# Optimization experiments

Hardware: AMD Instinct MI355X
Metric: run time of the kernel (lower is better)

The kernel has to match this reference:

```python
import jax, jax.numpy as jnp
import numpy as np

B, C, H, W = 8, 256, 128, 128
KC, VC, HEADS = 256, 256, 8


def setup_inputs() -> dict:
    key = jax.random.key(0)
    ks = jax.random.split(key, 10)
    s = 0.05
    return {
        "x": jax.random.normal(ks[0], (B, C, H, W), jnp.float32),
        "Wk": jax.random.normal(ks[1], (KC, C), jnp.float32) * s,
        "bk": jax.random.normal(ks[2], (KC,), jnp.float32) * s,
        "Wq": jax.random.normal(ks[3], (KC, C), jnp.float32) * s,
        "bq": jax.random.normal(ks[4], (KC,), jnp.float32) * s,
        "Wv": jax.random.normal(ks[5], (VC, C), jnp.float32) * s,
        "bv": jax.random.normal(ks[6], (VC,), jnp.float32) * s,
        "Wr": jax.random.normal(ks[7], (C, VC), jnp.float32) * s,
        "br": jax.random.normal(ks[8], (C,), jnp.float32) * s,
        "head_count": HEADS,
    }


def reference(x, Wk, bk, Wq, bq, Wv, bv, Wr, br, head_count):
    n, c, h, w = x.shape
    hw = h * w
    xf = x.reshape(n, c, hw)  # [n, C, S]
    # 1x1 convs == per-pixel linear projections
    keys = jnp.einsum('kc,ncs->nks', Wk, xf) + bk[None, :, None]
    queries = jnp.einsum('kc,ncs->nks', Wq, xf) + bq[None, :, None]
    values = jnp.einsum('vc,ncs->nvs', Wv, xf) + bv[None, :, None]

    dk = Wk.shape[0] // head_count
    dv = Wv.shape[0] // head_count
    # split heads along channel dim (matches torch channel slicing)
    K = jax.nn.softmax(keys.reshape(n, head_count, dk, hw), axis=-1)   # softmax over spatial
    Q = jax.nn.softmax(queries.reshape(n, head_count, dk, hw), axis=2) # softmax over key dim
    V = values.reshape(n, head_count, dv, hw)

    # context = K @ V^T : [n, h, dk, dv]
    ctx = jnp.einsum('nhks,nhvs->nhkv', K, V)
    # attended = ctx^T @ Q : [n, h, dv, S]
    att = jnp.einsum('nhkv,nhks->nhvs', ctx, Q).reshape(n, head_count * dv, h, w)

    attention = jnp.einsum('ov,nvhw->nohw', Wr, att) + br[None, :, None, None]
    # attention map: per-head mean over key dim, then mean over heads
    attention_map = K.mean(axis=2).mean(axis=1).reshape(n, h, w)
    # torch returns the LAST head's context (loop variable after the loop)
    context_last = ctx[:, -1]
    return attention, context_last, attention_map
```

## Files before the change

### kernel.cpp

```cpp
#include <hip/hip_runtime.h>
#include <hip/hip_bf16.h>

typedef float f32x4 __attribute__((ext_vector_type(4)));
typedef short s16x8 __attribute__((ext_vector_type(8)));
typedef __bf16 bf16x8 __attribute__((ext_vector_type(8)));
typedef unsigned short u16;

#define DEVI __device__ __forceinline__

static constexpr int    HW      = 16384;
static constexpr size_t BSTRIDE = (size_t)256 * HW;

static constexpr size_t oXBT   = 0;
static constexpr size_t oEK    = oXBT  + (size_t)8 * HW * 256 * 2;
static constexpr size_t oQT    = oEK   + (size_t)8 * 256 * HW * 2;
static constexpr size_t oVB    = oQT   + (size_t)8 * HW * 256 * 2;
static constexpr size_t oWK    = oVB   + (size_t)8 * 256 * HW * 2;
static constexpr size_t oBIAS  = oWK   + (size_t)768 * 256 * 2;
static constexpr size_t oISE   = oBIAS + 4096;
static constexpr size_t oPS    = oISE  + 8192;
static constexpr size_t oCTX   = oPS   + (size_t)256 * 2048 * 4;
static constexpr size_t oMB    = oCTX  + (size_t)64 * 1024 * 4;
static constexpr size_t oCPART = oMB   + (size_t)8 * 256 * 256 * 2;
static constexpr size_t oMPART = oCPART + (size_t)4096 * 1024 * 4;

DEVI float bf2f(short x) {
  unsigned u = ((unsigned)(unsigned short)x) << 16;
  return __builtin_bit_cast(float, u);
}
DEVI u16 f2bf(float x) { return __builtin_bit_cast(u16, (__bf16)x); }

DEVI void gld16(const void* g, void* l) {
  __builtin_amdgcn_global_load_lds(
      (__attribute__((address_space(1))) void*)(g),
      (__attribute__((address_space(3))) void*)(l), 16, 0, 0);
}

__global__ __launch_bounds__(256) void k_prep(
    const float* __restrict__ Wk, const float* __restrict__ Wq, const float* __restrict__ Wv,
    const float* __restrict__ bk, const float* __restrict__ bq, const float* __restrict__ bv,
    u16* __restrict__ Wkqv, float* __restrict__ bias)
{
  int i = blockIdx.x * 256 + threadIdx.x;
  for (int p = i; p < 768 * 256; p += 64 * 256) {
    float v = (p < 65536) ? Wk[p] : (p < 131072 ? Wq[p - 65536] : Wv[p - 131072]);
    Wkqv[p] = f2bf(v);
  }
  if (i < 768) bias[i] = (i < 256) ? bk[i] : (i < 512 ? bq[i - 256] : bv[i - 512]);
}

__global__ __launch_bounds__(256) void k_transpose(const float* __restrict__ in_, u16* __restrict__ out)
{
  __shared__ u16 lds[64 * 256];
  const int t = threadIdx.x;
  const int n = blockIdx.y;
  const int s0 = blockIdx.x * 64;
  const float* src = in_ + ((size_t)n * 256 + t) * HW + s0;
  #pragma unroll
  for (int i = 0; i < 16; ++i) {
    f32x4 v = *(const f32x4*)(src + i * 4);
    #pragma unroll
    for (int j = 0; j < 4; ++j) lds[(i * 4 + j) * 256 + t] = f2bf(v[j]);
  }
  __syncthreads();
  s16x8* gp = (s16x8*)(out + (size_t)n * BSTRIDE + (size_t)s0 * 256);
  const s16x8* lp = (const s16x8*)lds;
  #pragma unroll
  for (int i = 0; i < 8; ++i) gp[t + i * 256] = lp[t + i * 256];
}

__global__ __launch_bounds__(256) void k_proj(
    const u16* __restrict__ W, const u16* __restrict__ xbT, const float* __restrict__ bias,
    u16* __restrict__ ek, u16* __restrict__ qT, u16* __restrict__ vb, float* __restrict__ ps)
{
  __shared__ u16 smem[17408];
  u16* Al = smem;
  u16* Bl = smem + 8192;
  const int t = threadIdx.x;
  const int L = blockIdx.x;
  const int n  = L & 7;
  const int idx = L >> 3;
  const int mb = idx % 6;
  const int sb = idx / 6;
  const int m0 = mb * 128, s0 = sb * 128;
  const int lane = t & 63;
  const int l15 = lane & 15, l4 = lane >> 4;
  const int wv = t >> 6;
  const int wm = (wv & 1) * 64, wn = (wv >> 1) * 64;
  const u16* Ab = W + (size_t)m0 * 256;
  const u16* Bb = xbT + (size_t)n * BSTRIDE + (size_t)s0 * 256;
  const int ar = t >> 2, ac = (t & 3) * 8;

  f32x4 acc[4][4] = {};

  auto stage = [&](int buf, int k0) {
    gld16(Ab + (size_t)ar * 256 + k0 + ac,        Al + buf * 4096 + t * 8);
    gld16(Ab + (size_t)(ar + 64) * 256 + k0 + ac, Al + buf * 4096 + 2048 + t * 8);
    gld16(Bb + (size_t)ar * 256 + k0 + ac,        Bl + buf * 4096 + t * 8);
    gld16(Bb + (size_t)(ar + 64) * 256 + k0 + ac, Bl + buf * 4096 + 2048 + t * 8);
  };

  stage(0, 0);
  __syncthreads();
  #pragma unroll
  for (int kt = 0; kt < 8; ++kt) {
    const int buf = kt & 1;
    if (kt < 7) stage(buf ^ 1, (kt + 1) * 32);
    bf16x8 af[4], bff[4];
    #pragma unroll
    for (int g = 0; g < 4; ++g) {
      af[g]  = *(const bf16x8*)&Al[buf * 4096 + (wm + g * 16 + l15) * 32 + l4 * 8];
      bff[g] = *(const bf16x8*)&Bl[buf * 4096 + (wn + g * 16 + l15) * 32 + l4 * 8];
    }
    #pragma unroll
    for (int mg = 0; mg < 4; ++mg)
      #pragma unroll
      for (int ng = 0; ng < 4; ++ng)
        acc[mg][ng] = __builtin_amdgcn_mfma_f32_16x16x32_bf16(af[mg], bff[ng], acc[mg][ng], 0, 0, 0);
    __syncthreads();
  }

  #pragma unroll
  for (int mg = 0; mg < 4; ++mg)
    #pragma unroll
    for (int r = 0; r < 4; ++r) {
      const float bb = bias[m0 + wm + mg * 16 + l4 * 4 + r];
      #pragma unroll
      for (int ng = 0; ng < 4; ++ng) acc[mg][ng][r] += bb;
    }

  const int rowBase = (mb & 1) * 128;

  if (mb < 2) {
    #pragma unroll
    for (int mg = 0; mg < 4; ++mg)
      #pragma unroll
      for (int r = 0; r < 4; ++r) {
        float s_ = 0.f;
        #pragma unroll
        for (int ng = 0; ng < 4; ++ng) {
          const float e = __expf(acc[mg][ng][r]);
          acc[mg][ng][r] = e; s_ += e;
        }
        s_ += __shfl_xor(s_, 1); s_ += __shfl_xor(s_, 2);
        s_ += __shfl_xor(s_, 4); s_ += __shfl_xor(s_, 8);
        if (l15 == 0) {
          const int row = rowBase + wm + mg * 16 + l4 * 4 + r;
          ps[((size_t)(sb * 2 + (wn >> 6))) * 2048 + n * 256 + row] = s_;
        }
      }
    u16* O = ek + (size_t)n * BSTRIDE;
    #pragma unroll
    for (int mg = 0; mg < 4; ++mg)
      #pragma unroll
      for (int r = 0; r < 4; ++r) {
        const size_t row = rowBase + wm + mg * 16 + l4 * 4 + r;
        u16* op = O + row * HW + s0 + wn + l15;
        #pragma unroll
        for (int ng = 0; ng < 4; ++ng) op[ng * 16] = f2bf(acc[mg][ng][r]);
      }
  } else if (mb < 4) {
    #pragma unroll
    for (int hh = 0; hh < 2; ++hh)
      #pragma unroll
      for (int ng = 0; ng < 4; ++ng) {
        float s = 0.f;
        #pragma unroll
        for (int mg = hh * 2; mg < hh * 2 + 2; ++mg)
          #pragma unroll
          for (int r = 0; r < 4; ++r) { const float e = __expf(acc[mg][ng][r]); acc[mg][ng][r] = e; s += e; }
        s += __shfl_xor(s, 16);
        s += __shfl_xor(s, 32);
        const float inv = 1.f / s;
        #pragma unroll
        for (int mg = hh * 2; mg < hh * 2 + 2; ++mg)
          #pragma unroll
          for (int r = 0; r < 4; ++r) acc[mg][ng][r] *= inv;
      }
    #pragma unroll
    for (int mg = 0; mg < 4; ++mg)
      #pragma unroll
      for (int ng = 0; ng < 4; ++ng)
        #pragma unroll
        for (int r = 0; r < 4; ++r) {
          const int srow = wn + ng * 16 + l15;
          const int mcol = wm + mg * 16 + l4 * 4 + r;
          smem[srow * 136 + mcol] = f2bf(acc[mg][ng][r]);
        }
    __syncthreads();
    u16* O = qT + (size_t)n * BSTRIDE + (size_t)s0 * 256 + rowBase;
    #pragma unroll
    for (int it = 0; it < 8; ++it) {
      const int row = it * 16 + (t >> 4);
      *(s16x8*)(O + (size_t)row * 256 + (t & 15) * 8) = *(const s16x8*)&smem[row * 136 + (t & 15) * 8];
    }
  } else {
    u16* O = vb + (size_t)n * BSTRIDE;
    #pragma unroll
    for (int mg = 0; mg < 4; ++mg)
      #pragma unroll
      for (int r = 0; r < 4; ++r) {
        const size_t row = rowBase + wm + mg * 16 + l4 * 4 + r;
        u16* op = O + row * HW + s0 + wn + l15;
        #pragma unroll
        for (int ng = 0; ng < 4; ++ng) op[ng * 16] = f2bf(acc[mg][ng][r]);
      }
  }
}

__global__ __launch_bounds__(256) void k_inv(const float* __restrict__ ps, float* __restrict__ ise)
{
  const int i = blockIdx.x * 256 + threadIdx.x;
  float s = 0.f;
  for (int b = 0; b < 256; ++b) s += ps[(size_t)b * 2048 + i];
  ise[i] = 1.f / s;
}

__global__ __launch_bounds__(64) void k_ctx_part(
    const u16* __restrict__ ek, const u16* __restrict__ vb, const float* __restrict__ ise,
    float* __restrict__ cpart, float* __restrict__ mpart)
{
  const int blk = blockIdx.x;
  const int chunk = blk & 63, nh = blk >> 6;
  const int h = nh & 7, n = nh >> 3;
  const int lane = threadIdx.x;
  const int l15 = lane & 15, l4 = lane >> 4;
  const u16* kb = ek + ((size_t)n * 256 + h * 32) * HW;
  const u16* vv = vb + ((size_t)n * 256 + h * 32) * HW;
  const float iv0 = ise[n * 256 + h * 32 + l15];
  const float iv1 = ise[n * 256 + h * 32 + 16 + l15];
  f32x4 acc[2][2] = {};
  float macc[8][8] = {};
  const int sbase = chunk * 256 + l4 * 8;
  #pragma unroll
  for (int ks = 0; ks < 8; ++ks) {
    const int sb = sbase + ks * 32;
    bf16x8 ef[2], vf[2];
    #pragma unroll
    for (int g = 0; g < 2; ++g) {
      ef[g] = *(const bf16x8*)(kb + (size_t)(g * 16 + l15) * HW + sb);
// ... 50 lines not shown
  if (h == 7) *(f32x4*)(dctx + (size_t)n * 1024 + t * 4) = a;
}

__global__ __launch_bounds__(256) void k_mmat(
    const float* __restrict__ ctx, const float* __restrict__ Wr, u16* __restrict__ Mb)
{
  const int nh = blockIdx.x, n = nh >> 3, h = nh & 7, o = threadIdx.x;
  __shared__ float cl[1024];
  #pragma unroll
  for (int i = 0; i < 4; ++i) cl[o + i * 256] = ctx[(size_t)nh * 1024 + o + i * 256];
  __syncthreads();
  float wr[32];
  const float* wp = Wr + (size_t)o * 256 + h * 32;
  #pragma unroll
  for (int v = 0; v < 32; ++v) wr[v] = wp[v];
  u16* mp = Mb + ((size_t)n * 256 + o) * 256 + h * 32;
  #pragma unroll 4
  for (int k = 0; k < 32; ++k) {
    float s = 0.f;
    #pragma unroll
    for (int v = 0; v < 32; ++v) s += wr[v] * cl[k * 32 + v];
    mp[k] = f2bf(s);
  }
}

__global__ __launch_bounds__(256) void k_map_reduce(const float* __restrict__ mpart, float* __restrict__ dmap)
{
  const int i = blockIdx.x * 256 + threadIdx.x;
  f32x4 a = {};
  #pragma unroll
  for (int h = 0; h < 8; ++h) a += *(const f32x4*)(mpart + (size_t)h * 131072 + (size_t)i * 4);
  a *= (1.0f / 256.0f);
  *(f32x4*)(dmap + (size_t)i * 4) = a;
}

__global__ __launch_bounds__(256) void k_attn(
    const u16* __restrict__ Mb, const u16* __restrict__ qT, const float* __restrict__ br,
    float* __restrict__ Out)
{
  __shared__ u16 Al[2][4096];
  __shared__ u16 Bl[2][4096];
  const int t = threadIdx.x;
  const int L = blockIdx.x;
  const int n = L & 7;
  const int idx = L >> 3;
  const int m0 = (idx & 1) * 128;
  const int s0 = (idx >> 1) * 128;
  const int lane = t & 63;
  const int l15 = lane & 15, l4 = lane >> 4;
  const int wv = t >> 6;
  const int wm = (wv & 1) * 64, wn = (wv >> 1) * 64;
  const u16* Ab = Mb + (size_t)n * 65536 + (size_t)m0 * 256;
  const u16* Bb = qT + (size_t)n * BSTRIDE + (size_t)s0 * 256;
  const int ar = t >> 2, ac = (t & 3) * 8;

  f32x4 acc[4][4] = {};

  auto stage = [&](int buf, int k0) {
    gld16(Ab + (size_t)ar * 256 + k0 + ac,        &Al[buf][t * 8]);
    gld16(Ab + (size_t)(ar + 64) * 256 + k0 + ac, &Al[buf][2048 + t * 8]);
    gld16(Bb + (size_t)ar * 256 + k0 + ac,        &Bl[buf][t * 8]);
    gld16(Bb + (size_t)(ar + 64) * 256 + k0 + ac, &Bl[buf][2048 + t * 8]);
  };

  stage(0, 0);
  __syncthreads();
  #pragma unroll
  for (int kt = 0; kt < 8; ++kt) {
    const int buf = kt & 1;
    if (kt < 7) stage(buf ^ 1, (kt + 1) * 32);
    bf16x8 af[4], bff[4];
    #pragma unroll
    for (int g = 0; g < 4; ++g) {
      af[g]  = *(const bf16x8*)&Al[buf][(wm + g * 16 + l15) * 32 + l4 * 8];
      bff[g] = *(const bf16x8*)&Bl[buf][(wn + g * 16 + l15) * 32 + l4 * 8];
    }
    #pragma unroll
    for (int mg = 0; mg < 4; ++mg)
      #pragma unroll
      for (int ng = 0; ng < 4; ++ng)
        acc[mg][ng] = __builtin_amdgcn_mfma_f32_16x16x32_bf16(af[mg], bff[ng], acc[mg][ng], 0, 0, 0);
    __syncthreads();
  }

  float* O = Out + (size_t)n * BSTRIDE;
  #pragma unroll
  for (int mg = 0; mg < 4; ++mg)
    #pragma unroll
    for (int r = 0; r < 4; ++r) {
      const size_t row = m0 + wm + mg * 16 + l4 * 4 + r;
      const float bb = br[row];
      float* op = O + row * HW + s0 + wn + l15;
      #pragma unroll
      for (int ng = 0; ng < 4; ++ng) op[ng * 16] = acc[mg][ng][r] + bb;
    }
}

extern "C" void kernel_launch(void* const* d_in, const int* in_sizes, int n_in,
                              void* d_out, int out_size, void* d_ws, size_t ws_size,
                              hipStream_t stream)
{
  (void)in_sizes; (void)n_in; (void)out_size; (void)ws_size;
  const float* x  = (const float*)d_in[0];
  const float* Wk = (const float*)d_in[1];
  const float* bk = (const float*)d_in[2];
  const float* Wq = (const float*)d_in[3];
  const float* bq = (const float*)d_in[4];
  const float* Wv = (const float*)d_in[5];
  const float* bv = (const float*)d_in[6];
  const float* Wr = (const float*)d_in[7];
  const float* br = (const float*)d_in[8];

  char* ws = (char*)d_ws;
  u16*   xbT  = (u16*)(ws + oXBT);
  u16*   ek   = (u16*)(ws + oEK);
  u16*   qT   = (u16*)(ws + oQT);
  u16*   vb   = (u16*)(ws + oVB);
  u16*   Wkqv = (u16*)(ws + oWK);
  float* bias = (float*)(ws + oBIAS);
  float* ise  = (float*)(ws + oISE);
  float* ps   = (float*)(ws + oPS);
  float* ctx  = (float*)(ws + oCTX);
  u16*   Mb   = (u16*)(ws + oMB);
  float* cpart= (float*)(ws + oCPART);
  float* mpart= (float*)(ws + oMPART);

  float* attn = (float*)d_out;
  float* dctx = (float*)d_out + 33554432;
  float* dmap = (float*)d_out + 33562624;

  k_prep<<<64, 256, 0, stream>>>(Wk, Wq, Wv, bk, bq, bv, Wkqv, bias);
  k_transpose<<<dim3(256, 8), 256, 0, stream>>>(x, xbT);
  k_proj<<<6144, 256, 0, stream>>>(Wkqv, xbT, bias, ek, qT, vb, ps);
  k_inv<<<8, 256, 0, stream>>>(ps, ise);
  k_ctx_part<<<4096, 64, 0, stream>>>(ek, vb, ise, cpart, mpart);
  k_ctx_reduce<<<64, 256, 0, stream>>>(cpart, ise, ctx, dctx);
  k_mmat<<<64, 256, 0, stream>>>(ctx, Wr, Mb);
  k_map_reduce<<<128, 256, 0, stream>>>(mpart, dmap);
  k_attn<<<2048, 256, 0, stream>>>(Mb, qT, br, attn);
}
```

Measured before the change: 289.7 us.

## Replace projection and output GEMMs with 256x256-tile templated kernel with swizzled LDS

```diff
diff --git a/kernel.cpp b/kernel.cpp
--- a/kernel.cpp
+++ b/kernel.cpp
@@ -3,6 +3,7 @@
 
 typedef float f32x4 __attribute__((ext_vector_type(4)));
 typedef short s16x8 __attribute__((ext_vector_type(8)));
+typedef short s16x4 __attribute__((ext_vector_type(4)));
 typedef __bf16 bf16x8 __attribute__((ext_vector_type(8)));
 typedef unsigned short u16;
 
@@ -36,6 +37,8 @@
       (__attribute__((address_space(3))) void*)(l), 16, 0, 0);
 }
 
+DEVI void cfence() { asm volatile("" ::: "memory"); }
+
 __global__ __launch_bounds__(256) void k_prep(
     const float* __restrict__ Wk, const float* __restrict__ Wq, const float* __restrict__ Wv,
     const float* __restrict__ bk, const float* __restrict__ bq, const float* __restrict__ bv,
@@ -69,142 +72,186 @@
   for (int i = 0; i < 8; ++i) gp[t + i * 256] = lp[t + i * 256];
 }
 
-__global__ __launch_bounds__(256) void k_proj(
-    const u16* __restrict__ W, const u16* __restrict__ xbT, const float* __restrict__ bias,
-    u16* __restrict__ ek, u16* __restrict__ qT, u16* __restrict__ vb, float* __restrict__ ps)
-{
-  __shared__ u16 smem[17408];
-  u16* Al = smem;
-  u16* Bl = smem + 8192;
+template<int MODE>
+__global__ __launch_bounds__(512, 2) void k_gemm256(
+    const u16* __restrict__ A, const u16* __restrict__ B, const float* __restrict__ bias,
+    u16* __restrict__ o_ek, u16* __restrict__ o_qT, u16* __restrict__ o_vb,
+    float* __restrict__ o_ps, float* __restrict__ o_f32)
+{
+  __shared__ u16 smem[65536];
   const int t = threadIdx.x;
   const int L = blockIdx.x;
-  const int n  = L & 7;
+  const int n = L & 7;
   const int idx = L >> 3;
-  const int mb = idx % 6;
-  const int sb = idx / 6;
-  const int m0 = mb * 128, s0 = sb * 128;
+  int mb, sb;
+  if constexpr (MODE == 0) { mb = idx % 3; sb = idx / 3; }
+  else                     { mb = 0;       sb = idx; }
+  const int s0 = sb * 256;
   const int lane = t & 63;
   const int l15 = lane & 15, l4 = lane >> 4;
-  const int wv = t >> 6;
-  const int wm = (wv & 1) * 64, wn = (wv >> 1) * 64;
-  const u16* Ab = W + (size_t)m0 * 256;
-  const u16* Bb = xbT + (size_t)n * BSTRIDE + (size_t)s0 * 256;
-  const int ar = t >> 2, ac = (t & 3) * 8;
-
-  f32x4 acc[4][4] = {};
-
-  auto stage = [&](int buf, int k0) {
-    gld16(Ab + (size_t)ar * 256 + k0 + ac,        Al + buf * 4096 + t * 8);
-    gld16(Ab + (size_t)(ar + 64) * 256 + k0 + ac, Al + buf * 4096 + 2048 + t * 8);
-    gld16(Bb + (size_t)ar * 256 + k0 + ac,        Bl + buf * 4096 + t * 8);
-    gld16(Bb + (size_t)(ar + 64) * 256 + k0 + ac, Bl + buf * 4096 + 2048 + t * 8);
+  const int w = t >> 6;
+  const int wr = w & 1, wc = w >> 1;
+  const int tr = t >> 3;
+  const int csw = (t & 7) ^ (tr & 7);
+
+  const u16* Ag = A + (MODE == 0 ? (size_t)mb * 65536 : (size_t)n * 65536);
+  const u16* Bg = B + (size_t)n * BSTRIDE + (size_t)s0 * 256;
+
+  auto STAGE = [&](int buf, int kt) {
+    const int k0 = kt * 64 + csw * 8;
+    #pragma unroll
+    for (int i = 0; i < 4; ++i) {
+      const size_t r = (size_t)(i * 64 + tr);
+      gld16(Ag + r * 256 + k0, smem + buf * 16384 + (i * 512 + t) * 8);
+      gld16(Bg + r * 256 + k0, smem + 32768 + buf * 16384 + (i * 512 + t) * 8);
+    }
   };
 
-  stage(0, 0);
+  f32x4 acc[8][4] = {};
+
+  auto COMPUTE = [&](int buf) {
+    const u16* Al = smem + buf * 16384;
+    const u16* Bl = smem + 32768 + buf * 16384;
+    bf16x8 bf[4][2];
+    #pragma unroll
+    for (int b = 0; b < 4; ++b) {
+      const int s = wc * 64 + b * 16 + l15;
+      #pragma unroll
+      for (int ks = 0; ks < 2; ++ks)
+        bf[b][ks] = *(const bf16x8*)&Bl[s * 64 + ((ks * 4 + l4) ^ (s & 7)) * 8];
+    }
+    #pragma unroll
+    for (int p = 0; p < 4; ++p) {
+      bf16x8 af[2][2];
+      #pragma unroll
+      for (int a2 = 0; a2 < 2; ++a2) {
+        const int m = wr * 128 + (p * 2 + a2) * 16 + l15;
+        #pragma unroll
+        for (int ks = 0; ks < 2; ++ks)
+          af[a2][ks] = *(const bf16x8*)&Al[m * 64 + ((ks * 4 + l4) ^ (m & 7)) * 8];
+      }
+      __builtin_amdgcn_s_setprio(1);
+      #pragma unroll
+      for (int a2 = 0; a2 < 2; ++a2)
+        #pragma unroll
+        for (int b = 0; b < 4; ++b)
+          #pragma unroll
+          for (int ks = 0; ks < 2; ++ks)
+            acc[p * 2 + a2][b] = __builtin_amdgcn_mfma_f32_16x16x32_bf16(
+                af[a2][ks], bf[b][ks], acc[p * 2 + a2][b], 0, 0, 0);
+      __builtin_amdgcn_s_setprio(0);
+    }
+  };
+
+  STAGE(0, 0); STAGE(1, 1);
+  #pragma unroll
+  for (int kt = 0; kt < 4; ++kt) {
+    if (kt < 3) asm volatile("s_waitcnt vmcnt(8)" ::: "memory");
+    else        asm volatile("s_waitcnt vmcnt(0)" ::: "memory");
+    cfence(); __builtin_amdgcn_s_barrier(); cfence();
+    COMPUTE(kt & 1);
+    asm volatile("s_waitcnt lgkmcnt(0)" ::: "memory");
+    cfence(); __builtin_amdgcn_s_barrier(); cfence();
+    if (kt < 2) STAGE(kt & 1, kt + 2);
+  }
   __syncthreads();
-  #pragma unroll
-  for (int kt = 0; kt < 8; ++kt) {
-    const int buf = kt & 1;
-    if (kt < 7) stage(buf ^ 1, (kt + 1) * 32);
-    bf16x8 af[4], bff[4];
-    #pragma unroll
-    for (int g = 0; g < 4; ++g) {
-      af[g]  = *(const bf16x8*)&Al[buf * 4096 + (wm + g * 16 + l15) * 32 + l4 * 8];
-      bff[g] = *(const bf16x8*)&Bl[buf * 4096 + (wn + g * 16 + l15) * 32 + l4 * 8];
-    }
-    #pragma unroll
-    for (int mg = 0; mg < 4; ++mg)
-      #pragma unroll
-      for (int ng = 0; ng < 4; ++ng)
-        acc[mg][ng] = __builtin_amdgcn_mfma_f32_16x16x32_bf16(af[mg], bff[ng], acc[mg][ng], 0, 0, 0);
-    __syncthreads();
-  }
-
-  #pragma unroll
-  for (int mg = 0; mg < 4; ++mg)
-    #pragma unroll
-    for (int r = 0; r < 4; ++r) {
-      const float bb = bias[m0 + wm + mg * 16 + l4 * 4 + r];
-      #pragma unroll
-      for (int ng = 0; ng < 4; ++ng) acc[mg][ng][r] += bb;
-    }
-
-  const int rowBase = (mb & 1) * 128;
-
-  if (mb < 2) {
-    #pragma unroll
-    for (int mg = 0; mg < 4; ++mg)
+
+  if constexpr (MODE == 1) {
+    float* O = o_f32 + (size_t)n * BSTRIDE;
+    #pragma unroll
+    for (int am = 0; am < 8; ++am)
       #pragma unroll
       for (int r = 0; r < 4; ++r) {
-        float s_ = 0.f;
-        #pragma unroll
-        for (int ng = 0; ng < 4; ++ng) {
-          const float e = __expf(acc[mg][ng][r]);
-          acc[mg][ng][r] = e; s_ += e;
-        }
+        const int m = wr * 128 + am * 16 + l4 * 4 + r;
+        const float bb = bias[m];
+        float* op = O + (size_t)m * HW + s0 + wc * 64 + l15;
+        #pragma unroll
+        for (int b = 0; b < 4; ++b) op[b * 16] = acc[am][b][r] + bb;
+      }
+    return;
+  } else {
+  if (mb == 0) {
+    float* psrow = o_ps + ((size_t)(sb * 4 + wc) * 8 + n) * 256;
+    u16* O = o_ek + (size_t)n * BSTRIDE;
+    #pragma unroll
+    for (int am = 0; am < 8; ++am)
+      #pragma unroll
+      for (int r = 0; r < 4; ++r) {
+        const int m = wr * 128 + am * 16 + l4 * 4 + r;
+        const float bb = bias[m];
+        const float e0 = __expf(acc[am][0][r] + bb), e1 = __expf(acc[am][1][r] + bb);
+        const float e2 = __expf(acc[am][2][r] + bb), e3 = __expf(acc[am][3][r] + bb);
+        float s_ = e0 + e1 + e2 + e3;
         s_ += __shfl_xor(s_, 1); s_ += __shfl_xor(s_, 2);
         s_ += __shfl_xor(s_, 4); s_ += __shfl_xor(s_, 8);
-        if (l15 == 0) {
-          const int row = rowBase + wm + mg * 16 + l4 * 4 + r;
-          ps[((size_t)(sb * 2 + (wn >> 6))) * 2048 + n * 256 + row] = s_;
-        }
-      }
-    u16* O = ek + (size_t)n * BSTRIDE;
-    #pragma unroll
-    for (int mg = 0; mg < 4; ++mg)
+        if (l15 == 0) psrow[m] = s_;
+        u16* op = O + (size_t)m * HW + s0 + wc * 64 + l15;
+        op[0] = f2bf(e0); op[16] = f2bf(e1); op[32] = f2bf(e2); op[48] = f2bf(e3);
+      }
+  } else if (mb == 1) {
+    #pragma unroll
+    for (int am = 0; am < 8; ++am)
       #pragma unroll
       for (int r = 0; r < 4; ++r) {
-        const size_t row = rowBase + wm + mg * 16 + l4 * 4 + r;
-        u16* op = O + row * HW + s0 + wn + l15;
-        #pragma unroll
-        for (int ng = 0; ng < 4; ++ng) op[ng * 16] = f2bf(acc[mg][ng][r]);
-      }
-  } else if (mb < 4) {
-    #pragma unroll
-    for (int hh = 0; hh < 2; ++hh)
-      #pragma unroll
-      for (int ng = 0; ng < 4; ++ng) {
+        const float bb = bias[256 + wr * 128 + am * 16 + l4 * 4 + r];
+        #pragma unroll
+        for (int b = 0; b < 4; ++b) acc[am][b][r] += bb;
+      }
+    #pragma unroll
+    for (int hh = 0; hh < 4; ++hh)
+      #pragma unroll
+      for (int b = 0; b < 4; ++b) {
         float s = 0.f;
         #pragma unroll
-        for (int mg = hh * 2; mg < hh * 2 + 2; ++mg)
+        for (int a2 = 0; a2 < 2; ++a2)
           #pragma unroll
-          for (int r = 0; r < 4; ++r) { const float e = __expf(acc[mg][ng][r]); acc[mg][ng][r] = e; s += e; }
-        s += __shfl_xor(s, 16);
-        s += __shfl_xor(s, 32);
+          for (int r = 0; r < 4; ++r) {
+            const float e = __expf(acc[hh * 2 + a2][b][r]);
+            acc[hh * 2 + a2][b][r] = e; s += e;
+          }
+        s += __shfl_xor(s, 16); s += __shfl_xor(s, 32);
         const float inv = 1.f / s;
         #pragma unroll
-        for (int mg = hh * 2; mg < hh * 2 + 2; ++mg)
+        for (int a2 = 0; a2 < 2; ++a2)
           #pragma unroll
-          for (int r = 0; r < 4; ++r) acc[mg][ng][r] *= inv;
-      }
-    #pragma unroll
-    for (int mg = 0; mg < 4; ++mg)
-      #pragma unroll
-      for (int ng = 0; ng < 4; ++ng)
-        #pragma unroll
-        for (int r = 0; r < 4; ++r) {
-          const int srow = wn + ng * 16 + l15;
-          const int mcol = wm + mg * 16 + l4 * 4 + r;
-          smem[srow * 136 + mcol] = f2bf(acc[mg][ng][r]);
-        }
-    __syncthreads();
-    u16* O = qT + (size_t)n * BSTRIDE + (size_t)s0 * 256 + rowBase;
-    #pragma unroll
-    for (int it = 0; it < 8; ++it) {
-      const int row = it * 16 + (t >> 4);
-      *(s16x8*)(O + (size_t)row * 256 + (t & 15) * 8) = *(const s16x8*)&smem[row * 136 + (t & 15) * 8];
+          for (int r = 0; r < 4; ++r) acc[hh * 2 + a2][b][r] *= inv;
+      }
+    #pragma unroll
+    for (int H = 0; H < 2; ++H) {
+      if ((wc >> 1) == H) {
+        #pragma unroll
+        for (int am = 0; am < 8; ++am)
+          #pragma unroll
+          for (int b = 0; b < 4; ++b) {
+            const int srow = wc * 64 + b * 16 + l15 - H * 128;
+            s16x4 pk;
+            #pragma unroll
+            for (int r = 0; r < 4; ++r) pk[r] = (short)f2bf(acc[am][b][r]);
+            *(s16x4*)&smem[srow * 264 + wr * 128 + am * 16 + l4 * 4] = pk;
+          }
+      }
+      __syncthreads();
+      const int row = t >> 2;
+      const int cq = (t & 3) * 64;
+      u16* dst = o_qT + (size_t)n * BSTRIDE + (size_t)(s0 + H * 128 + row) * 256 + cq;
+      const u16* srcl = smem + row * 264 + cq;
+      #pragma unroll
+      for (int i = 0; i < 8; ++i) *(s16x8*)(dst + i * 8) = *(const s16x8*)(srcl + i * 8);
+      __syncthreads();
     }
   } else {
-    u16* O = vb + (size_t)n * BSTRIDE;
-    #pragma unroll
-    for (int mg = 0; mg < 4; ++mg)
+    u16* O = o_vb + (size_t)n * BSTRIDE;
+    #pragma unroll
+    for (int am = 0; am < 8; ++am)
       #pragma unroll
       for (int r = 0; r < 4; ++r) {
-        const size_t row = rowBase + wm + mg * 16 + l4 * 4 + r;
-        u16* op = O + row * HW + s0 + wn + l15;
-        #pragma unroll
-        for (int ng = 0; ng < 4; ++ng) op[ng * 16] = f2bf(acc[mg][ng][r]);
-      }
+        const int m = wr * 128 + am * 16 + l4 * 4 + r;
+        const float bb = bias[512 + m];
+        u16* op = O + (size_t)m * HW + s0 + wc * 64 + l15;
+        #pragma unroll
+        for (int b = 0; b < 4; ++b) op[b * 16] = f2bf(acc[am][b][r] + bb);
+      }
+  }
   }
 }
 
@@ -322,68 +369,6 @@
   for (int h = 0; h < 8; ++h) a += *(const f32x4*)(mpart + (size_t)h * 131072 + (size_t)i * 4);
   a *= (1.0f / 256.0f);
   *(f32x4*)(dmap + (size_t)i * 4) = a;
-}
-
-__global__ __launch_bounds__(256) void k_attn(
-    const u16* __restrict__ Mb, const u16* __restrict__ qT, const float* __restrict__ br,
-    float* __restrict__ Out)
-{
-  __shared__ u16 Al[2][4096];
-  __shared__ u16 Bl[2][4096];
-  const int t = threadIdx.x;
-  const int L = blockIdx.x;
-  const int n = L & 7;
-  const int idx = L >> 3;
-  const int m0 = (idx & 1) * 128;
-  const int s0 = (idx >> 1) * 128;
-  const int lane = t & 63;
-  const int l15 = lane & 15, l4 = lane >> 4;
-  const int wv = t >> 6;
-  const int wm = (wv & 1) * 64, wn = (wv >> 1) * 64;
-  const u16* Ab = Mb + (size_t)n * 65536 + (size_t)m0 * 256;
-  const u16* Bb = qT + (size_t)n * BSTRIDE + (size_t)s0 * 256;
-  const int ar = t >> 2, ac = (t & 3) * 8;
-
-  f32x4 acc[4][4] = {};
-
-  auto stage = [&](int buf, int k0) {
-    gld16(Ab + (size_t)ar * 256 + k0 + ac,        &Al[buf][t * 8]);
-    gld16(Ab + (size_t)(ar + 64) * 256 + k0 + ac, &Al[buf][2048 + t * 8]);
-    gld16(Bb + (size_t)ar * 256 + k0 + ac,        &Bl[buf][t * 8]);
-    gld16(Bb + (size_t)(ar + 64) * 256 + k0 + ac, &Bl[buf][2048 + t * 8]);
-  };
-
-  stage(0, 0);
-  __syncthreads();
-  #pragma unroll
-  for (int kt = 0; kt < 8; ++kt) {
-    const int buf = kt & 1;
-    if (kt < 7) stage(buf ^ 1, (kt + 1) * 32);
-    bf16x8 af[4], bff[4];
-    #pragma unroll
-    for (int g = 0; g < 4; ++g) {
-      af[g]  = *(const bf16x8*)&Al[buf][(wm + g * 16 + l15) * 32 + l4 * 8];
-      bff[g] = *(const bf16x8*)&Bl[buf][(wn + g * 16 + l15) * 32 + l4 * 8];
-    }
-    #pragma unroll
-    for (int mg = 0; mg < 4; ++mg)
-      #pragma unroll
-      for (int ng = 0; ng < 4; ++ng)
-        acc[mg][ng] = __builtin_amdgcn_mfma_f32_16x16x32_bf16(af[mg], bff[ng], acc[mg][ng], 0, 0, 0);
-    __syncthreads();
-  }
-
-  float* O = Out + (size_t)n * BSTRIDE;
-  #pragma unroll
-  for (int mg = 0; mg < 4; ++mg)
-    #pragma unroll
-    for (int r = 0; r < 4; ++r) {
-      const size_t row = m0 + wm + mg * 16 + l4 * 4 + r;
-      const float bb = br[row];
-      float* op = O + row * HW + s0 + wn + l15;
-      #pragma unroll
-      for (int ng = 0; ng < 4; ++ng) op[ng * 16] = acc[mg][ng][r] + bb;
-    }
 }
 
 extern "C" void kernel_launch(void* const* d_in, const int* in_sizes, int n_in,
@@ -421,11 +406,11 @@
 
   k_prep<<<64, 256, 0, stream>>>(Wk, Wq, Wv, bk, bq, bv, Wkqv, bias);
   k_transpose<<<dim3(256, 8), 256, 0, stream>>>(x, xbT);
-  k_proj<<<6144, 256, 0, stream>>>(Wkqv, xbT, bias, ek, qT, vb, ps);
+  k_gemm256<0><<<1536, 512, 0, stream>>>(Wkqv, xbT, bias, ek, qT, vb, ps, nullptr);
   k_inv<<<8, 256, 0, stream>>>(ps, ise);
   k_ctx_part<<<4096, 64, 0, stream>>>(ek, vb, ise, cpart, mpart);
   k_ctx_reduce<<<64, 256, 0, stream>>>(cpart, ise, ctx, dctx);
   k_mmat<<<64, 256, 0, stream>>>(ctx, Wr, Mb);
   k_map_reduce<<<128, 256, 0, stream>>>(mpart, dmap);
-  k_attn<<<2048, 256, 0, stream>>>(Mb, qT, br, attn);
-}
+  k_gemm256<1><<<512, 512, 0, stream>>>(Mb, qT, br, nullptr, nullptr, nullptr, nullptr, attn);
+}
```

Measured after the change: 316.6 us. 1.09x slower.

## Unify projection and output GEMMs into persistent multi-tile kernel with swizzled LDS

Applied to the files above, without the earlier changes.

```diff
diff --git a/kernel.cpp b/kernel.cpp
--- a/kernel.cpp
+++ b/kernel.cpp
@@ -3,6 +3,7 @@
 
 typedef float f32x4 __attribute__((ext_vector_type(4)));
 typedef short s16x8 __attribute__((ext_vector_type(8)));
+typedef short s16x4 __attribute__((ext_vector_type(4)));
 typedef __bf16 bf16x8 __attribute__((ext_vector_type(8)));
 typedef unsigned short u16;
 
@@ -36,6 +37,8 @@
       (__attribute__((address_space(3))) void*)(l), 16, 0, 0);
 }
 
+DEVI void cfence() { asm volatile("" ::: "memory"); }
+
 __global__ __launch_bounds__(256) void k_prep(
     const float* __restrict__ Wk, const float* __restrict__ Wq, const float* __restrict__ Wv,
     const float* __restrict__ bk, const float* __restrict__ bq, const float* __restrict__ bv,
@@ -49,162 +52,189 @@
   if (i < 768) bias[i] = (i < 256) ? bk[i] : (i < 512 ? bq[i - 256] : bv[i - 512]);
 }
 
-__global__ __launch_bounds__(256) void k_transpose(const float* __restrict__ in_, u16* __restrict__ out)
-{
-  __shared__ u16 lds[64 * 256];
+__global__ __launch_bounds__(256) void k_transpose(const float* __restrict__ x, u16* __restrict__ out)
+{
+  __shared__ u16 T[64 * 264];
   const int t = threadIdx.x;
   const int n = blockIdx.y;
   const int s0 = blockIdx.x * 64;
-  const float* src = in_ + ((size_t)n * 256 + t) * HW + s0;
+  const int cg = t >> 4;
+  const int sl = (t & 15) * 4;
   #pragma unroll
   for (int i = 0; i < 16; ++i) {
-    f32x4 v = *(const f32x4*)(src + i * 4);
-    #pragma unroll
-    for (int j = 0; j < 4; ++j) lds[(i * 4 + j) * 256 + t] = f2bf(v[j]);
+    const int c = i * 16 + cg;
+    f32x4 v = *(const f32x4*)(x + ((size_t)n * 256 + c) * HW + s0 + sl);
+    #pragma unroll
+    for (int j = 0; j < 4; ++j) T[(sl + j) * 264 + c] = f2bf(v[j]);
   }
   __syncthreads();
-  s16x8* gp = (s16x8*)(out + (size_t)n * BSTRIDE + (size_t)s0 * 256);
-  const s16x8* lp = (const s16x8*)lds;
-  #pragma unroll
-  for (int i = 0; i < 8; ++i) gp[t + i * 256] = lp[t + i * 256];
-}
-
-__global__ __launch_bounds__(256) void k_proj(
-    const u16* __restrict__ W, const u16* __restrict__ xbT, const float* __restrict__ bias,
-    u16* __restrict__ ek, u16* __restrict__ qT, u16* __restrict__ vb, float* __restrict__ ps)
-{
-  __shared__ u16 smem[17408];
+  const int sr = t >> 2, ch = (t & 3) * 64;
+  u16* dst = out + (size_t)n * BSTRIDE + (size_t)(s0 + sr) * 256 + ch;
+  const u16* srcl = &T[sr * 264 + ch];
+  #pragma unroll
+  for (int i = 0; i < 8; ++i) *(s16x8*)(dst + i * 8) = *(const s16x8*)(srcl + i * 8);
+}
+
+template<int MODE>
+__global__ __launch_bounds__(256, 4) void k_gemm2(
+    const u16* __restrict__ A, const u16* __restrict__ B, const float* __restrict__ bias,
+    u16* __restrict__ o_ek, u16* __restrict__ o_qT, u16* __restrict__ o_vb,
+    float* __restrict__ o_ps, float* __restrict__ o_f32)
+{
+  __shared__ u16 smem[16384];
+  const int t = threadIdx.x;
+  const int L = blockIdx.x;
+  const int n = L & 7;
+  const int idx = L >> 3;
+  int mb, sq;
+  if constexpr (MODE == 0) { mb = idx % 6; sq = idx / 6; }
+  else                     { mb = idx & 1; sq = idx >> 1; }
+  const int m0 = mb * 128;
+  const int lane = t & 63;
+  const int l15 = lane & 15, l4 = (lane >> 4) & 3;
+  const int wv = t >> 6;
+  const int wm = (wv & 1) * 64, wn = (wv >> 1) * 64;
+  const u16* Ab = A + ((MODE == 0) ? (size_t)0 : (size_t)n * 65536) + (size_t)m0 * 256;
+  const u16* Bb = B + (size_t)n * BSTRIDE;
+  const int ar = t >> 2;
+  const int acs = (((t & 3) ^ (ar & 3)) * 8);
+
   u16* Al = smem;
   u16* Bl = smem + 8192;
-  const int t = threadIdx.x;
-  const int L = blockIdx.x;
-  const int n  = L & 7;
-  const int idx = L >> 3;
-  const int mb = idx % 6;
-  const int sb = idx / 6;
-  const int m0 = mb * 128, s0 = sb * 128;
-  const int lane = t & 63;
-  const int l15 = lane & 15, l4 = lane >> 4;
-  const int wv = t >> 6;
-  const int wm = (wv & 1) * 64, wn = (wv >> 1) * 64;
-  const u16* Ab = W + (size_t)m0 * 256;
-  const u16* Bb = xbT + (size_t)n * BSTRIDE + (size_t)s0 * 256;
-  const int ar = t >> 2, ac = (t & 3) * 8;
+
+  auto STAGE = [&](int it) {
+    const int buf = it & 1;
+    const int k0 = (it & 7) * 32;
+    const size_t srow = (size_t)((sq * 4 + (it >> 3)) * 128);
+    gld16(Ab + (size_t)ar * 256 + k0 + acs,          Al + buf * 4096 + t * 8);
+    gld16(Ab + (size_t)(ar + 64) * 256 + k0 + acs,   Al + buf * 4096 + 2048 + t * 8);
+    gld16(Bb + (srow + ar) * 256 + k0 + acs,         Bl + buf * 4096 + t * 8);
+    gld16(Bb + (srow + ar + 64) * 256 + k0 + acs,    Bl + buf * 4096 + 2048 + t * 8);
+  };
 
   f32x4 acc[4][4] = {};
-
-  auto stage = [&](int buf, int k0) {
-    gld16(Ab + (size_t)ar * 256 + k0 + ac,        Al + buf * 4096 + t * 8);
-    gld16(Ab + (size_t)(ar + 64) * 256 + k0 + ac, Al + buf * 4096 + 2048 + t * 8);
-    gld16(Bb + (size_t)ar * 256 + k0 + ac,        Bl + buf * 4096 + t * 8);
-    gld16(Bb + (size_t)(ar + 64) * 256 + k0 + ac, Bl + buf * 4096 + 2048 + t * 8);
-  };
-
-  stage(0, 0);
-  __syncthreads();
-  #pragma unroll
-  for (int kt = 0; kt < 8; ++kt) {
-    const int buf = kt & 1;
-    if (kt < 7) stage(buf ^ 1, (kt + 1) * 32);
+  STAGE(0);
+
+  u16* ekb = (MODE == 0) ? o_ek + (size_t)n * BSTRIDE : nullptr;
+  u16* vbb = (MODE == 0) ? o_vb + (size_t)n * BSTRIDE : nullptr;
+  u16* qtb = (MODE == 0) ? o_qT + (size_t)n * BSTRIDE : nullptr;
+  float* ob = (MODE == 1) ? o_f32 + (size_t)n * BSTRIDE : nullptr;
+
+  #pragma unroll 8
+  for (int it = 0; it < 32; ++it) {
+    if (it < 31) {
+      STAGE(it + 1);
+      asm volatile("s_waitcnt vmcnt(4)" ::: "memory");
+    } else {
+      asm volatile("s_waitcnt vmcnt(0)" ::: "memory");
+    }
+    cfence(); __builtin_amdgcn_s_barrier(); cfence();
+
+    const int buf = it & 1;
     bf16x8 af[4], bff[4];
     #pragma unroll
     for (int g = 0; g < 4; ++g) {
-      af[g]  = *(const bf16x8*)&Al[buf * 4096 + (wm + g * 16 + l15) * 32 + l4 * 8];
-      bff[g] = *(const bf16x8*)&Bl[buf * 4096 + (wn + g * 16 + l15) * 32 + l4 * 8];
-    }
+      const int mrow = wm + g * 16 + l15;
+      const int srw  = wn + g * 16 + l15;
+      af[g]  = *(const bf16x8*)&Al[buf * 4096 + mrow * 32 + ((l4 ^ (l15 & 3)) * 8)];
+      bff[g] = *(const bf16x8*)&Bl[buf * 4096 + srw  * 32 + ((l4 ^ (l15 & 3)) * 8)];
+    }
+    __builtin_amdgcn_s_setprio(1);
     #pragma unroll
     for (int mg = 0; mg < 4; ++mg)
       #pragma unroll
       for (int ng = 0; ng < 4; ++ng)
         acc[mg][ng] = __builtin_amdgcn_mfma_f32_16x16x32_bf16(af[mg], bff[ng], acc[mg][ng], 0, 0, 0);
-    __syncthreads();
-  }
-
-  #pragma unroll
-  for (int mg = 0; mg < 4; ++mg)
-    #pragma unroll
-    for (int r = 0; r < 4; ++r) {
-      const float bb = bias[m0 + wm + mg * 16 + l4 * 4 + r];
+    __builtin_amdgcn_s_setprio(0);
+
+    asm volatile("s_waitcnt lgkmcnt(0)" ::: "memory");
+    cfence(); __builtin_amdgcn_s_barrier(); cfence();
+
+    if ((it & 7) == 7) {
+      const int tile = it >> 3;
+      const int s0t = (sq * 4 + tile) * 128;
+      if constexpr (MODE == 1) {
+        #pragma unroll
+        for (int mg = 0; mg < 4; ++mg)
+          #pragma unroll
+          for (int r = 0; r < 4; ++r) {
+            const int m = m0 + wm + mg * 16 + l4 * 4 + r;
+            const float bb = bias[m];
+            float* op = ob + (size_t)m * HW + s0t + wn + l15;
+            #pragma unroll
+            for (int ng = 0; ng < 4; ++ng) op[ng * 16] = acc[mg][ng][r] + bb;
+          }
+      } else if (mb < 2) {
+        const int stile = sq * 4 + tile;
+        #pragma unroll
+        for (int mg = 0; mg < 4; ++mg)
+          #pragma unroll
+          for (int r = 0; r < 4; ++r) {
+            const int m = m0 + wm + mg * 16 + l4 * 4 + r;
+            const float bb = bias[m];
+            float e[4], s_ = 0.f;
+            #pragma unroll
+            for (int ng = 0; ng < 4; ++ng) { e[ng] = __expf(acc[mg][ng][r] + bb); s_ += e[ng]; }
+            s_ += __shfl_xor(s_, 1); s_ += __shfl_xor(s_, 2);
+            s_ += __shfl_xor(s_, 4); s_ += __shfl_xor(s_, 8);
+            if (l15 == 0)
+              o_ps[((size_t)(stile * 2 + (wn >> 6))) * 2048 + n * 256 + m] = s_;
+            u16* op = ekb + (size_t)m * HW + s0t + wn + l15;
+            #pragma unroll
+            for (int ng = 0; ng < 4; ++ng) op[ng * 16] = f2bf(e[ng]);
+          }
+      } else if (mb < 4) {
+        #pragma unroll
+        for (int mg = 0; mg < 4; ++mg)
+          #pragma unroll
+          for (int r = 0; r < 4; ++r) {
+            const float bb = bias[m0 + wm + mg * 16 + l4 * 4 + r];
+            #pragma unroll
+            for (int ng = 0; ng < 4; ++ng) acc[mg][ng][r] += bb;
+          }
+        #pragma unroll
+        for (int hh = 0; hh < 2; ++hh)
+          #pragma unroll
+          for (int ng = 0; ng < 4; ++ng) {
+            float s = 0.f;
+            #pragma unroll
+            for (int mg = hh * 2; mg < hh * 2 + 2; ++mg)
+              #pragma unroll
+              for (int r = 0; r < 4; ++r) { const float e = __expf(acc[mg][ng][r]); acc[mg][ng][r] = e; s += e; }
+            s += __shfl_xor(s, 16); s += __shfl_xor(s, 32);
+            const float inv = 1.f / s;
+            #pragma unroll
+            for (int mg = hh * 2; mg < hh * 2 + 2; ++mg)
+              #pragma unroll
+              for (int r = 0; r < 4; ++r) acc[mg][ng][r] *= inv;
+          }
+        const int mcb = (m0 - 256) + wm;
+        #pragma unroll
+        for (int mg = 0; mg < 4; ++mg)
+          #pragma unroll
+          for (int ng = 0; ng < 4; ++ng) {
+            s16x4 pk;
+            #pragma unroll
+            for (int r = 0; r < 4; ++r) pk[r] = (short)f2bf(acc[mg][ng][r]);
+            *(s16x4*)(qtb + (size_t)(s0t + wn + ng * 16 + l15) * 256 + mcb + mg * 16 + l4 * 4) = pk;
+          }
+      } else {
+        #pragma unroll
+        for (int mg = 0; mg < 4; ++mg)
+          #pragma unroll
+          for (int r = 0; r < 4; ++r) {
+            const int m = m0 + wm + mg * 16 + l4 * 4 + r;
+            const float bb = bias[m];
+            u16* op = vbb + (size_t)(m - 512) * HW + s0t + wn + l15;
+            #pragma unroll
+            for (int ng = 0; ng < 4; ++ng) op[ng * 16] = f2bf(acc[mg][ng][r] + bb);
+          }
+      }
       #pragma unroll
-      for (int ng = 0; ng < 4; ++ng) acc[mg][ng][r] += bb;
-    }
-
-  const int rowBase = (mb & 1) * 128;
-
-  if (mb < 2) {
-    #pragma unroll
-    for (int mg = 0; mg < 4; ++mg)
-      #pragma unroll
-      for (int r = 0; r < 4; ++r) {
-        float s_ = 0.f;
-        #pragma unroll
-        for (int ng = 0; ng < 4; ++ng) {
-          const float e = __expf(acc[mg][ng][r]);
-          acc[mg][ng][r] = e; s_ += e;
-        }
-        s_ += __shfl_xor(s_, 1); s_ += __shfl_xor(s_, 2);
-        s_ += __shfl_xor(s_, 4); s_ += __shfl_xor(s_, 8);
-        if (l15 == 0) {
-          const int row = rowBase + wm + mg * 16 + l4 * 4 + r;
-          ps[((size_t)(sb * 2 + (wn >> 6))) * 2048 + n * 256 + row] = s_;
-        }
-      }
-    u16* O = ek + (size_t)n * BSTRIDE;
-    #pragma unroll
-    for (int mg = 0; mg < 4; ++mg)
-      #pragma unroll
-      for (int r = 0; r < 4; ++r) {
-        const size_t row = rowBase + wm + mg * 16 + l4 * 4 + r;
-        u16* op = O + row * HW + s0 + wn + l15;
-        #pragma unroll
-        for (int ng = 0; ng < 4; ++ng) op[ng * 16] = f2bf(acc[mg][ng][r]);
-      }
-  } else if (mb < 4) {
-    #pragma unroll
-    for (int hh = 0; hh < 2; ++hh)
-      #pragma unroll
-      for (int ng = 0; ng < 4; ++ng) {
-        float s = 0.f;
-        #pragma unroll
-        for (int mg = hh * 2; mg < hh * 2 + 2; ++mg)
-          #pragma unroll
-          for (int r = 0; r < 4; ++r) { const float e = __expf(acc[mg][ng][r]); acc[mg][ng][r] = e; s += e; }
-        s += __shfl_xor(s, 16);
-        s += __shfl_xor(s, 32);
-        const float inv = 1.f / s;
-        #pragma unroll
-        for (int mg = hh * 2; mg < hh * 2 + 2; ++mg)
-          #pragma unroll
-          for (int r = 0; r < 4; ++r) acc[mg][ng][r] *= inv;
-      }
-    #pragma unroll
-    for (int mg = 0; mg < 4; ++mg)
-      #pragma unroll
-      for (int ng = 0; ng < 4; ++ng)
-        #pragma unroll
-        for (int r = 0; r < 4; ++r) {
-          const int srow = wn + ng * 16 + l15;
-          const int mcol = wm + mg * 16 + l4 * 4 + r;
-          smem[srow * 136 + mcol] = f2bf(acc[mg][ng][r]);
-        }
-    __syncthreads();
-    u16* O = qT + (size_t)n * BSTRIDE + (size_t)s0 * 256 + rowBase;
-    #pragma unroll
-    for (int it = 0; it < 8; ++it) {
-      const int row = it * 16 + (t >> 4);
-      *(s16x8*)(O + (size_t)row * 256 + (t & 15) * 8) = *(const s16x8*)&smem[row * 136 + (t & 15) * 8];
-    }
-  } else {
-    u16* O = vb + (size_t)n * BSTRIDE;
-    #pragma unroll
-    for (int mg = 0; mg < 4; ++mg)
-      #pragma unroll
-      for (int r = 0; r < 4; ++r) {
-        const size_t row = rowBase + wm + mg * 16 + l4 * 4 + r;
-        u16* op = O + row * HW + s0 + wn + l15;
-        #pragma unroll
-        for (int ng = 0; ng < 4; ++ng) op[ng * 16] = f2bf(acc[mg][ng][r]);
-      }
+      for (int mg = 0; mg < 4; ++mg)
+        #pragma unroll
+        for (int ng = 0; ng < 4; ++ng) acc[mg][ng] = f32x4{0.f, 0.f, 0.f, 0.f};
+    }
   }
 }
 
@@ -322,68 +352,6 @@
   for (int h = 0; h < 8; ++h) a += *(const f32x4*)(mpart + (size_t)h * 131072 + (size_t)i * 4);
   a *= (1.0f / 256.0f);
   *(f32x4*)(dmap + (size_t)i * 4) = a;
-}
-
-__global__ __launch_bounds__(256) void k_attn(
-    const u16* __restrict__ Mb, const u16* __restrict__ qT, const float* __restrict__ br,
-    float* __restrict__ Out)
-{
-  __shared__ u16 Al[2][4096];
-  __shared__ u16 Bl[2][4096];
-  const int t = threadIdx.x;
-  const int L = blockIdx.x;
-  const int n = L & 7;
-  const int idx = L >> 3;
-  const int m0 = (idx & 1) * 128;
-  const int s0 = (idx >> 1) * 128;
-  const int lane = t & 63;
-  const int l15 = lane & 15, l4 = lane >> 4;
-  const int wv = t >> 6;
-  const int wm = (wv & 1) * 64, wn = (wv >> 1) * 64;
-  const u16* Ab = Mb + (size_t)n * 65536 + (size_t)m0 * 256;
-  const u16* Bb = qT + (size_t)n * BSTRIDE + (size_t)s0 * 256;
-  const int ar = t >> 2, ac = (t & 3) * 8;
-
-  f32x4 acc[4][4] = {};
-
-  auto stage = [&](int buf, int k0) {
-    gld16(Ab + (size_t)ar * 256 + k0 + ac,        &Al[buf][t * 8]);
-    gld16(Ab + (size_t)(ar + 64) * 256 + k0 + ac, &Al[buf][2048 + t * 8]);
-    gld16(Bb + (size_t)ar * 256 + k0 + ac,        &Bl[buf][t * 8]);
-    gld16(Bb + (size_t)(ar + 64) * 256 + k0 + ac, &Bl[buf][2048 + t * 8]);
-  };
-
-  stage(0, 0);
-  __syncthreads();
-  #pragma unroll
-  for (int kt = 0; kt < 8; ++kt) {
-    const int buf = kt & 1;
-    if (kt < 7) stage(buf ^ 1, (kt + 1) * 32);
-    bf16x8 af[4], bff[4];
-    #pragma unroll
-    for (int g = 0; g < 4; ++g) {
-      af[g]  = *(const bf16x8*)&Al[buf][(wm + g * 16 + l15) * 32 + l4 * 8];
-      bff[g] = *(const bf16x8*)&Bl[buf][(wn + g * 16 + l15) * 32 + l4 * 8];
-    }
-    #pragma unroll
-    for (int mg = 0; mg < 4; ++mg)
-      #pragma unroll
-      for (int ng = 0; ng < 4; ++ng)
-        acc[mg][ng] = __builtin_amdgcn_mfma_f32_16x16x32_bf16(af[mg], bff[ng], acc[mg][ng], 0, 0, 0);
-    __syncthreads();
-  }
-
-  float* O = Out + (size_t)n * BSTRIDE;
-  #pragma unroll
-  for (int mg = 0; mg < 4; ++mg)
-    #pragma unroll
-    for (int r = 0; r < 4; ++r) {
-      const size_t row = m0 + wm + mg * 16 + l4 * 4 + r;
-      const float bb = br[row];
-      float* op = O + row * HW + s0 + wn + l15;
-      #pragma unroll
-      for (int ng = 0; ng < 4; ++ng) op[ng * 16] = acc[mg][ng][r] + bb;
-    }
 }
 
 extern "C" void kernel_launch(void* const* d_in, const int* in_sizes, int n_in,
@@ -421,11 +389,11 @@
 
   k_prep<<<64, 256, 0, stream>>>(Wk, Wq, Wv, bk, bq, bv, Wkqv, bias);
   k_transpose<<<dim3(256, 8), 256, 0, stream>>>(x, xbT);
-  k_proj<<<6144, 256, 0, stream>>>(Wkqv, xbT, bias, ek, qT, vb, ps);
+  k_gemm2<0><<<1536, 256, 0, stream>>>(Wkqv, xbT, bias, ek, qT, vb, ps, nullptr);
   k_inv<<<8, 256, 0, stream>>>(ps, ise);
   k_ctx_part<<<4096, 64, 0, stream>>>(ek, vb, ise, cpart, mpart);
   k_ctx_reduce<<<64, 256, 0, stream>>>(cpart, ise, ctx, dctx);
   k_mmat<<<64, 256, 0, stream>>>(ctx, Wr, Mb);
   k_map_reduce<<<128, 256, 0, stream>>>(mpart, dmap);
-  k_attn<<<2048, 256, 0, stream>>>(Mb, qT, br, attn);
-}
+  k_gemm2<1><<<512, 256, 0, stream>>>(Mb, qT, br, nullptr, nullptr, nullptr, nullptr, attn);
+}
```

New measurement: 508.3 us (median of 2 runs). 75.5% more time.

## Rework GEMM mainloop with BK=64, XOR-swizzled LDS and vmcnt-based prefetch

Applied to the files above, without the earlier changes.

```diff
diff --git a/kernel.cpp b/kernel.cpp
--- a/kernel.cpp
+++ b/kernel.cpp
@@ -3,6 +3,7 @@
 
 typedef float f32x4 __attribute__((ext_vector_type(4)));
 typedef short s16x8 __attribute__((ext_vector_type(8)));
+typedef short s16x4 __attribute__((ext_vector_type(4)));
 typedef __bf16 bf16x8 __attribute__((ext_vector_type(8)));
 typedef unsigned short u16;
 
@@ -69,13 +70,56 @@
   for (int i = 0; i < 8; ++i) gp[t + i * 256] = lp[t + i * 256];
 }
 
-__global__ __launch_bounds__(256) void k_proj(
+
+#define GEMM_CORE(Ab, Bb)                                                                   \
+  u16* Al = smem;                                                                           \
+  u16* Bl = smem + 16384;                                                                   \
+  auto STAGE = [&](int buf, int kt) {                                                       \
+    const int k0 = kt * 64;                                                                 \
+    _Pragma("unroll")                                                                       \
+    for (int i = 0; i < 4; ++i) {                                                           \
+      const int r_ = i * 32 + (t >> 3);                                                     \
+      const int cs = (((t & 7) ^ (r_ & 7)) * 8);                                            \
+      gld16((Ab) + (size_t)r_ * 256 + k0 + cs, Al + buf * 8192 + i * 2048 + t * 8);         \
+      gld16((Bb) + (size_t)r_ * 256 + k0 + cs, Bl + buf * 8192 + i * 2048 + t * 8);         \
+    }                                                                                       \
+  };                                                                                        \
+  f32x4 acc[4][4] = {};                                                                     \
+  STAGE(0, 0); STAGE(1, 1);                                                                 \
+  _Pragma("unroll")                                                                         \
+  for (int kt = 0; kt < 4; ++kt) {                                                          \
+    if (kt < 3) asm volatile("s_waitcnt vmcnt(8)" ::: "memory");                            \
+    else        asm volatile("s_waitcnt vmcnt(0)" ::: "memory");                            \
+    __builtin_amdgcn_s_barrier();                                                           \
+    const int buf = kt & 1;                                                                 \
+    _Pragma("unroll")                                                                       \
+    for (int ks = 0; ks < 2; ++ks) {                                                        \
+      bf16x8 af[4], bff[4];                                                                 \
+      _Pragma("unroll")                                                                     \
+      for (int g = 0; g < 4; ++g) {                                                         \
+        const int mrow = wm + g * 16 + l15;                                                 \
+        const int srow = wn + g * 16 + l15;                                                 \
+        af[g]  = *(const bf16x8*)&Al[buf * 8192 + mrow * 64 + (((ks * 4 + l4) ^ (mrow & 7)) * 8)]; \
+        bff[g] = *(const bf16x8*)&Bl[buf * 8192 + srow * 64 + (((ks * 4 + l4) ^ (srow & 7)) * 8)]; \
+      }                                                                                     \
+      __builtin_amdgcn_s_setprio(1);                                                        \
+      _Pragma("unroll")                                                                     \
+      for (int mg = 0; mg < 4; ++mg)                                                        \
+        _Pragma("unroll")                                                                   \
+        for (int ng = 0; ng < 4; ++ng)                                                      \
+          acc[mg][ng] = __builtin_amdgcn_mfma_f32_16x16x32_bf16(af[mg], bff[ng], acc[mg][ng], 0, 0, 0); \
+      __builtin_amdgcn_s_setprio(0);                                                        \
+    }                                                                                       \
+    asm volatile("s_waitcnt lgkmcnt(0)" ::: "memory");                                      \
+    __builtin_amdgcn_s_barrier();                                                           \
+    if (kt < 2) STAGE(buf, kt + 2);                                                         \
+  }
+
+__global__ __launch_bounds__(256, 2) void k_proj(
     const u16* __restrict__ W, const u16* __restrict__ xbT, const float* __restrict__ bias,
     u16* __restrict__ ek, u16* __restrict__ qT, u16* __restrict__ vb, float* __restrict__ ps)
 {
-  __shared__ u16 smem[17408];
-  u16* Al = smem;
-  u16* Bl = smem + 8192;
+  __shared__ u16 smem[32768];
   const int t = threadIdx.x;
   const int L = blockIdx.x;
   const int n  = L & 7;
@@ -84,41 +128,13 @@
   const int sb = idx / 6;
   const int m0 = mb * 128, s0 = sb * 128;
   const int lane = t & 63;
-  const int l15 = lane & 15, l4 = lane >> 4;
+  const int l15 = lane & 15, l4 = (lane >> 4) & 3;
   const int wv = t >> 6;
   const int wm = (wv & 1) * 64, wn = (wv >> 1) * 64;
   const u16* Ab = W + (size_t)m0 * 256;
   const u16* Bb = xbT + (size_t)n * BSTRIDE + (size_t)s0 * 256;
-  const int ar = t >> 2, ac = (t & 3) * 8;
-
-  f32x4 acc[4][4] = {};
-
-  auto stage = [&](int buf, int k0) {
-    gld16(Ab + (size_t)ar * 256 + k0 + ac,        Al + buf * 4096 + t * 8);
-    gld16(Ab + (size_t)(ar + 64) * 256 + k0 + ac, Al + buf * 4096 + 2048 + t * 8);
-    gld16(Bb + (size_t)ar * 256 + k0 + ac,        Bl + buf * 4096 + t * 8);
-    gld16(Bb + (size_t)(ar + 64) * 256 + k0 + ac, Bl + buf * 4096 + 2048 + t * 8);
-  };
-
-  stage(0, 0);
-  __syncthreads();
-  #pragma unroll
-  for (int kt = 0; kt < 8; ++kt) {
-    const int buf = kt & 1;
-    if (kt < 7) stage(buf ^ 1, (kt + 1) * 32);
-    bf16x8 af[4], bff[4];
-    #pragma unroll
-    for (int g = 0; g < 4; ++g) {
-      af[g]  = *(const bf16x8*)&Al[buf * 4096 + (wm + g * 16 + l15) * 32 + l4 * 8];
-      bff[g] = *(const bf16x8*)&Bl[buf * 4096 + (wn + g * 16 + l15) * 32 + l4 * 8];
-    }
-    #pragma unroll
-    for (int mg = 0; mg < 4; ++mg)
-      #pragma unroll
-      for (int ng = 0; ng < 4; ++ng)
-        acc[mg][ng] = __builtin_amdgcn_mfma_f32_16x16x32_bf16(af[mg], bff[ng], acc[mg][ng], 0, 0, 0);
-    __syncthreads();
-  }
+
+  GEMM_CORE(Ab, Bb)
 
   #pragma unroll
   for (int mg = 0; mg < 4; ++mg)
@@ -177,6 +193,7 @@
           #pragma unroll
           for (int r = 0; r < 4; ++r) acc[mg][ng][r] *= inv;
       }
+    __syncthreads();
     #pragma unroll
     for (int mg = 0; mg < 4; ++mg)
       #pragma unroll
@@ -206,6 +223,39 @@
         for (int ng = 0; ng < 4; ++ng) op[ng * 16] = f2bf(acc[mg][ng][r]);
       }
   }
+}
+
+__global__ __launch_bounds__(256, 2) void k_attn(
+    const u16* __restrict__ Mb, const u16* __restrict__ qT, const float* __restrict__ br,
+    float* __restrict__ Out)
+{
+  __shared__ u16 smem[32768];
+  const int t = threadIdx.x;
+  const int L = blockIdx.x;
+  const int n = L & 7;
+  const int idx = L >> 3;
+  const int m0 = (idx & 1) * 128;
+  const int s0 = (idx >> 1) * 128;
+  const int lane = t & 63;
+  const int l15 = lane & 15, l4 = (lane >> 4) & 3;
+  const int wv = t >> 6;
+  const int wm = (wv & 1) * 64, wn = (wv >> 1) * 64;
+  const u16* Ab = Mb + (size_t)n * 65536 + (size_t)m0 * 256;
+  const u16* Bb = qT + (size_t)n * BSTRIDE + (size_t)s0 * 256;
+
+  GEMM_CORE(Ab, Bb)
+
+  float* O = Out + (size_t)n * BSTRIDE;
+  #pragma unroll
+  for (int mg = 0; mg < 4; ++mg)
+    #pragma unroll
+    for (int r = 0; r < 4; ++r) {
+      const size_t row = m0 + wm + mg * 16 + l4 * 4 + r;
+      const float bb = br[row];
+      float* op = O + row * HW + s0 + wn + l15;
+      #pragma unroll
+      for (int ng = 0; ng < 4; ++ng) op[ng * 16] = acc[mg][ng][r] + bb;
+    }
 }
 
 __global__ __launch_bounds__(256) void k_inv(const float* __restrict__ ps, float* __restrict__ ise)
@@ -322,68 +372,6 @@
   for (int h = 0; h < 8; ++h) a += *(const f32x4*)(mpart + (size_t)h * 131072 + (size_t)i * 4);
   a *= (1.0f / 256.0f);
   *(f32x4*)(dmap + (size_t)i * 4) = a;
-}
-
-__global__ __launch_bounds__(256) void k_attn(
-    const u16* __restrict__ Mb, const u16* __restrict__ qT, const float* __restrict__ br,
-    float* __restrict__ Out)
-{
-  __shared__ u16 Al[2][4096];
-  __shared__ u16 Bl[2][4096];
-  const int t = threadIdx.x;
-  const int L = blockIdx.x;
-  const int n = L & 7;
-  const int idx = L >> 3;
-  const int m0 = (idx & 1) * 128;
-  const int s0 = (idx >> 1) * 128;
-  const int lane = t & 63;
-  const int l15 = lane & 15, l4 = lane >> 4;
-  const int wv = t >> 6;
-  const int wm = (wv & 1) * 64, wn = (wv >> 1) * 64;
-  const u16* Ab = Mb + (size_t)n * 65536 + (size_t)m0 * 256;
-  const u16* Bb = qT + (size_t)n * BSTRIDE + (size_t)s0 * 256;
-  const int ar = t >> 2, ac = (t & 3) * 8;
-
-  f32x4 acc[4][4] = {};
-
-  auto stage = [&](int buf, int k0) {
-    gld16(Ab + (size_t)ar * 256 + k0 + ac,        &Al[buf][t * 8]);
-    gld16(Ab + (size_t)(ar + 64) * 256 + k0 + ac, &Al[buf][2048 + t * 8]);
-    gld16(Bb + (size_t)ar * 256 + k0 + ac,        &Bl[buf][t * 8]);
-    gld16(Bb + (size_t)(ar + 64) * 256 + k0 + ac, &Bl[buf][2048 + t * 8]);
-  };
-
-  stage(0, 0);
-  __syncthreads();
-  #pragma unroll
-  for (int kt = 0; kt < 8; ++kt) {
-    const int buf = kt & 1;
-    if (kt < 7) stage(buf ^ 1, (kt + 1) * 32);
-    bf16x8 af[4], bff[4];
-    #pragma unroll
-    for (int g = 0; g < 4; ++g) {
-      af[g]  = *(const bf16x8*)&Al[buf][(wm + g * 16 + l15) * 32 + l4 * 8];
-      bff[g] = *(const bf16x8*)&Bl[buf][(wn + g * 16 + l15) * 32 + l4 * 8];
-    }
-    #pragma unroll
-    for (int mg = 0; mg < 4; ++mg)
-      #pragma unroll
-      for (int ng = 0; ng < 4; ++ng)
-        acc[mg][ng] = __builtin_amdgcn_mfma_f32_16x16x32_bf16(af[mg], bff[ng], acc[mg][ng], 0, 0, 0);
-    __syncthreads();
-  }
-
-  float* O = Out + (size_t)n * BSTRIDE;
-  #pragma unroll
-  for (int mg = 0; mg < 4; ++mg)
-    #pragma unroll
-    for (int r = 0; r < 4; ++r) {
-      const size_t row = m0 + wm + mg * 16 + l4 * 4 + r;
-      const float bb = br[row];
-      float* op = O + row * HW + s0 + wn + l15;
-      #pragma unroll
-      for (int ng = 0; ng < 4; ++ng) op[ng * 16] = acc[mg][ng][r] + bb;
-    }
 }
 
 extern "C" void kernel_launch(void* const* d_in, const int* in_sizes, int n_in,
```

Result: no change. 287.1 us (-0.9%).
